# Kernel optimization log

Measured on AMD Instinct MI355X. Metric: run time of the kernel, lower is better.

## Reference

```python
import jax, jax.numpy as jnp
import numpy as np

D_MODEL = 1024
NUM_HEADS = 16
HEAD_DIM = D_MODEL // NUM_HEADS  # 64


def setup_inputs() -> dict:
    key = jax.random.key(0)
    ks = jax.random.split(key, 9)
    s = 1.0 / np.sqrt(D_MODEL)
    return {
        "x": jax.random.normal(ks[0], (2, 2048, D_MODEL), dtype=jnp.float32),
        "Wq": jax.random.normal(ks[1], (D_MODEL, D_MODEL), dtype=jnp.float32) * s,
        "bq": jnp.zeros((D_MODEL,), dtype=jnp.float32),
        "Wk": jax.random.normal(ks[2], (D_MODEL, HEAD_DIM), dtype=jnp.float32) * s,
        "bk": jnp.zeros((HEAD_DIM,), dtype=jnp.float32),
        "Wv": jax.random.normal(ks[3], (D_MODEL, HEAD_DIM), dtype=jnp.float32) * s,
        "bv": jnp.zeros((HEAD_DIM,), dtype=jnp.float32),
        "Wo": jax.random.normal(ks[4], (D_MODEL, D_MODEL), dtype=jnp.float32) * s,
        "bo": jnp.zeros((D_MODEL,), dtype=jnp.float32),
    }


def reference(x, Wq, bq, Wk, bk, Wv, bv, Wo, bo):
    B, S, D = x.shape
    H, hd = NUM_HEADS, HEAD_DIM
    # Projections: Q has H heads, K/V a single shared head (MQA).
    Q = (x @ Wq + bq).reshape(B, S, H, hd).transpose(0, 2, 1, 3)  # [B,H,S,hd]
    K = x @ Wk + bk  # [B,S,hd]
    V = x @ Wv + bv  # [B,S,hd]
    # Shared-K/V attention: broadcast K across heads instead of expand().
    scores = jnp.einsum("bhqd,bkd->bhqk", Q, K) / np.sqrt(hd)  # [B,H,S,S]
    attn = jax.nn.softmax(scores, axis=-1)
    attended = jnp.einsum("bhqk,bkd->bhqd", attn, V)  # [B,H,S,hd]
    attended = attended.transpose(0, 2, 1, 3).reshape(B, S, D)
    return attended @ Wo + bo
```

## Files before the change

kernel.cpp:

```cpp
#include <hip/hip_runtime.h>
#include <hip/hip_bf16.h>

#define D_MODEL 1024
#define NHEADS  16
#define HD      64
#define BATCH   2
#define SEQ     2048
#define MROWS   4096
#define NQKV    1152
#define NSPLIT  2

typedef short  short4v __attribute__((ext_vector_type(4)));
typedef short  short8  __attribute__((ext_vector_type(8)));
typedef float  floatx4 __attribute__((ext_vector_type(4)));

__device__ inline short f2bf(float f) {
  unsigned u = __builtin_bit_cast(unsigned, f);
  u = (u + 0x7FFF + ((u >> 16) & 1)) >> 16;
  return (short)u;
}

__device__ inline unsigned pack_trunc(float lo, float hi) {
  return __builtin_amdgcn_perm(__builtin_bit_cast(unsigned, hi),
                               __builtin_bit_cast(unsigned, lo), 0x07060302u);
}

__device__ inline void async_copy16(const short* g, short* l) {
  __builtin_amdgcn_global_load_lds(
      (const __attribute__((address_space(1))) unsigned int*)g,
      (__attribute__((address_space(3))) unsigned int*)l, 16, 0, 0);
}

__global__ __launch_bounds__(256)
void prep_kernel(const float* __restrict__ x,  const float* __restrict__ Wq,
                 const float* __restrict__ Wk, const float* __restrict__ Wv,
                 const float* __restrict__ Wo, const float* __restrict__ bq,
                 const float* __restrict__ bk, const float* __restrict__ bv,
                 short* __restrict__ xb, short* __restrict__ Wqkv_t,
                 short* __restrict__ Wo_t, float* __restrict__ bqkv) {
  const int id = blockIdx.x;
  const int t  = threadIdx.x;
  if (id < 544) {
    __shared__ short Ts[64 * 72];
    const float* src; short* dst; int N, off, tile;
    if (id < 256)      { src = Wq; dst = Wqkv_t; N = 1024; off = 0;    tile = id; }
    else if (id < 272) { src = Wk; dst = Wqkv_t; N = 64;   off = 1024; tile = id - 256; }
    else if (id < 288) { src = Wv; dst = Wqkv_t; N = 64;   off = 1088; tile = id - 272; }
    else               { src = Wo; dst = Wo_t;   N = 1024; off = 0;    tile = id - 288; }
    const int k0 = (N == 1024) ? (tile & 15) * 64 : tile * 64;
    const int n0 = (N == 1024) ? (tile >> 4) * 64 : 0;
    {
      const int r = t >> 2, c = (t & 3) * 16;
      const float* s = src + (size_t)(k0 + r) * N + n0 + c;
#pragma unroll
      for (int j = 0; j < 16; j += 4) {
        float4 v = *reinterpret_cast<const float4*>(s + j);
        Ts[r * 72 + c + j + 0] = f2bf(v.x); Ts[r * 72 + c + j + 1] = f2bf(v.y);
        Ts[r * 72 + c + j + 2] = f2bf(v.z); Ts[r * 72 + c + j + 3] = f2bf(v.w);
      }
    }
    __syncthreads();
    {
      const int n = t >> 2, kc = (t & 3) * 16;
      short8 o0, o1;
#pragma unroll
      for (int j = 0; j < 8; ++j) o0[j] = Ts[(kc + j) * 72 + n];
#pragma unroll
      for (int j = 0; j < 8; ++j) o1[j] = Ts[(kc + 8 + j) * 72 + n];
      short* d = dst + (size_t)(off + n0 + n) * 1024 + k0 + kc;
      *reinterpret_cast<short8*>(d)     = o0;
      *reinterpret_cast<short8*>(d + 8) = o1;
    }
  } else if (id < 549) {
    const int i = (id - 544) * 256 + t;
    if (i < 1024)      bqkv[i] = bq[i];
    else if (i < 1088) bqkv[i] = bk[i - 1024];
    else if (i < 1152) bqkv[i] = bv[i - 1088];
  } else {
    const int i = ((id - 549) * 256 + t) * 8;
    if (i < MROWS * D_MODEL) {
      float4 a = *reinterpret_cast<const float4*>(x + i);
      float4 b = *reinterpret_cast<const float4*>(x + i + 4);
      short8 o;
      o[0] = f2bf(a.x); o[1] = f2bf(a.y); o[2] = f2bf(a.z); o[3] = f2bf(a.w);
      o[4] = f2bf(b.x); o[5] = f2bf(b.y); o[6] = f2bf(b.z); o[7] = f2bf(b.w);
      *reinterpret_cast<short8*>(xb + i) = o;
    }
  }
}

template<bool OUT_BF16, int SCALE_N, bool VT_FUSE>
__global__ __launch_bounds__(256)
void gemm_mfma_bt(const short* __restrict__ A, const short* __restrict__ Bt,
                  const float* __restrict__ bias, void* __restrict__ Cout,
                  short* __restrict__ Vtg, int M, int N, int K) {
  __shared__ short As[128 * 64];
  __shared__ short Bs[64 * 64];
  const int t    = threadIdx.x;
  const int w    = t >> 6;
  const int lane = t & 63;
  const int quad = lane >> 4;
  const int l16  = lane & 15;
  const int bm   = blockIdx.x * 128;
  const int bn   = blockIdx.y * 64;
  const int wm   = (w >> 1) * 64;
  const int wn   = (w & 1) * 32;

  const int srow = t >> 3;
  const int cc   = ((t & 7) ^ (srow & 7)) * 8;
  const short* gA = A  + (size_t)(bm + srow) * K + cc;
  const short* gB = Bt + (size_t)(bn + srow) * K + cc;
  short* lA = As + t * 8;
  short* lB = Bs + t * 8;

  floatx4 acc[4][2];
#pragma unroll
  for (int i = 0; i < 4; ++i)
#pragma unroll
    for (int j = 0; j < 2; ++j) acc[i][j] = (floatx4){0.f, 0.f, 0.f, 0.f};

  const int xr = l16 & 7;

  for (int k0 = 0; k0 < K; k0 += 64) {
    __syncthreads();
    async_copy16(gA + k0, lA);
    async_copy16(gA + (size_t)32 * K + k0, lA + 2048);
    async_copy16(gA + (size_t)64 * K + k0, lA + 4096);
    async_copy16(gA + (size_t)96 * K + k0, lA + 6144);
    async_copy16(gB + k0, lB);
    async_copy16(gB + (size_t)32 * K + k0, lB + 2048);
    __syncthreads();

    short8 fa0[4], fa1[4], fb0[2], fb1[2];
#pragma unroll
    for (int mi = 0; mi < 4; ++mi) {
      const int row = wm + mi * 16 + l16;
      fa0[mi] = *reinterpret_cast<const short8*>(&As[row * 64 + (quad ^ xr) * 8]);
      fa1[mi] = *reinterpret_cast<const short8*>(&As[row * 64 + ((4 + quad) ^ xr) * 8]);
    }
#pragma unroll
    for (int ni = 0; ni < 2; ++ni) {
      const int row = wn + ni * 16 + l16;
      fb0[ni] = *reinterpret_cast<const short8*>(&Bs[row * 64 + (quad ^ xr) * 8]);
      fb1[ni] = *reinterpret_cast<const short8*>(&Bs[row * 64 + ((4 + quad) ^ xr) * 8]);
    }
#pragma unroll
    for (int mi = 0; mi < 4; ++mi)
#pragma unroll
      for (int ni = 0; ni < 2; ++ni) {
        acc[mi][ni] = __builtin_amdgcn_mfma_f32_16x16x32_bf16(fa0[mi], fb0[ni], acc[mi][ni], 0, 0, 0);
        acc[mi][ni] = __builtin_amdgcn_mfma_f32_16x16x32_bf16(fa1[mi], fb1[ni], acc[mi][ni], 0, 0, 0);
      }
  }

#pragma unroll
  for (int ni = 0; ni < 2; ++ni) {
    const int col = bn + wn + ni * 16 + l16;
    const float bs = bias[col];
    const float sc = (col < SCALE_N) ? 0.18033688f : 1.0f;
#pragma unroll
    for (int mi = 0; mi < 4; ++mi) {
      const int row = bm + wm + mi * 16 + quad * 4;
      short4v vt4;
#pragma unroll
      for (int r = 0; r < 4; ++r) {
        const float v = (acc[mi][ni][r] + bs) * sc;
        if (OUT_BF16) {
          const short bv16 = f2bf(v);
          ((short*)Cout)[(size_t)(row + r) * N + col] = bv16;
          if (VT_FUSE) vt4[r] = bv16;
        } else {
          ((float*)Cout)[(size_t)(row + r) * N + col] = v;
        }
      }
      if (VT_FUSE && col >= 1088) {
        const int d = col - 1088;
        const int b = row >> 11, s = row & 2047;
        *reinterpret_cast<short4v*>(&Vtg[(size_t)(b * 64 + d) * SEQ + s]) = vt4;
      }
    }
  }
}

__global__ __launch_bounds__(256, 3)
void mqa_flash_bf16(const short* __restrict__ QKV, const short* __restrict__ Vtg,
                    _Float16* __restrict__ Opart, float* __restrict__ lpart) {
  const int bh    = blockIdx.y;
  const int b     = bh >> 4;
  const int h     = bh & 15;
  const int s0    = blockIdx.x * 128;
  const int split = blockIdx.z;
  const int t     = threadIdx.x;
  const int w     = t >> 6;
  const int lane  = t & 63;
  const int quad  = lane >> 4;
  const int l16   = lane & 15;

  __shared__ short KVs[16384];
  __shared__ short Ps[4 * 16 * 64];
  short* myPs = Ps + w * 1024;

  short8 aq[2][2];
#pragma unroll
  for (int st = 0; st < 2; ++st) {
    const short* qrow = &QKV[(size_t)(b * SEQ + s0 + w * 32 + st * 16 + l16) * NQKV + h * HD];
    aq[st][0] = *reinterpret_cast<const short8*>(qrow + quad * 8);
    aq[st][1] = *reinterpret_cast<const short8*>(qrow + 32 + quad * 8);
  }

  floatx4 oacc[2][4];
  floatx4 lacc[2];
#pragma unroll
  for (int st = 0; st < 2; ++st) {
    lacc[st] = (floatx4){0.f, 0.f, 0.f, 0.f};
#pragma unroll
    for (int dg = 0; dg < 4; ++dg) oacc[st][dg] = (floatx4){0.f, 0.f, 0.f, 0.f};
  }

  short8 ones;
#pragma unroll
  for (int j = 0; j < 8; ++j) ones[j] = (short)0x3F80;

  const int srow  = t >> 3;
  const int cc    = ((t & 7) ^ (srow & 7)) * 8;
  const int kbase = split * (SEQ / NSPLIT);
  const short* gK = QKV + (size_t)(b * SEQ + kbase + srow) * NQKV + 1024 + cc;
  const short* gV = Vtg + (size_t)(b * 64 + srow) * SEQ + kbase + cc;
  short* lK = KVs + w * 512;
  short* lV = KVs + 4096 + w * 512;

  const int xr = l16 & 7;

  async_copy16(gK, lK);
  async_copy16(gK + (size_t)32 * NQKV, lK + 2048);
  async_copy16(gV, lV);
  async_copy16(gV + (size_t)32 * SEQ, lV + 2048);
  gK += (size_t)64 * NQKV;
  gV += 64;

  const int NT = (SEQ / NSPLIT) / 64;
  int cur = 0;

  for (int it = 0; it < NT; ++it) {
    asm volatile("s_waitcnt vmcnt(0)" ::: "memory");
    __builtin_amdgcn_s_barrier();
    __builtin_amdgcn_sched_barrier(0);

    if (it + 1 < NT) {
      const int nb = (cur ^ 1) * 8192;
      async_copy16(gK, lK + nb);
      async_copy16(gK + (size_t)32 * NQKV, lK + nb + 2048);
      async_copy16(gV, lV + nb);
      async_copy16(gV + (size_t)32 * SEQ, lV + nb + 2048);
      gK += (size_t)64 * NQKV;
      gV += 64;
    }

    const short* Ks = KVs + cur * 8192;
    const short* Vt = Ks + 4096;

    short8 kb[4][2], vb[4][2];
#pragma unroll
    for (int kg = 0; kg < 4; ++kg) {
      kb[kg][0] = *reinterpret_cast<const short8*>(&Ks[(kg * 16 + l16) * 64 + (quad ^ xr) * 8]);
      kb[kg][1] = *reinterpret_cast<const short8*>(&Ks[(kg * 16 + l16) * 64 + ((4 + quad) ^ xr) * 8]);
    }
#pragma unroll
    for (int dg = 0; dg < 4; ++dg) {
      vb[dg][0] = *reinterpret_cast<const short8*>(&Vt[(dg * 16 + l16) * 64 + (quad ^ xr) * 8]);
      vb[dg][1] = *reinterpret_cast<const short8*>(&Vt[(dg * 16 + l16) * 64 + ((4 + quad) ^ xr) * 8]);
    }
    asm volatile("s_waitcnt lgkmcnt(0)" ::: "memory");
    __builtin_amdgcn_sched_barrier(0);

#pragma unroll
    for (int st = 0; st < 2; ++st) {
#pragma unroll
      for (int kg = 0; kg < 4; ++kg) {
        floatx4 s4 = (floatx4){0.f, 0.f, 0.f, 0.f};
        s4 = __builtin_amdgcn_mfma_f32_16x16x32_bf16(kb[kg][0], aq[st][0], s4, 0, 0, 0);
        s4 = __builtin_amdgcn_mfma_f32_16x16x32_bf16(kb[kg][1], aq[st][1], s4, 0, 0, 0);
        float p0 = __builtin_exp2f(s4[0]);
        float p1 = __builtin_exp2f(s4[1]);
        float p2 = __builtin_exp2f(s4[2]);
        float p3 = __builtin_exp2f(s4[3]);
        uint2 pk;
        pk.x = pack_trunc(p0, p1);
        pk.y = pack_trunc(p2, p3);
        *reinterpret_cast<uint2*>(
            &myPs[l16 * 64 + (((2 * kg + (quad >> 1)) ^ xr) * 8) + (quad & 1) * 4]) = pk;
      }
      short8 ap0 = *reinterpret_cast<const short8*>(&myPs[l16 * 64 + ((quad ^ xr) * 8)]);
      short8 ap1 = *reinterpret_cast<const short8*>(&myPs[l16 * 64 + (((4 + quad) ^ xr) * 8)]);
      __builtin_amdgcn_s_setprio(1);
      lacc[st] = __builtin_amdgcn_mfma_f32_16x16x32_bf16(ap0, ones, lacc[st], 0, 0, 0);
      lacc[st] = __builtin_amdgcn_mfma_f32_16x16x32_bf16(ap1, ones, lacc[st], 0, 0, 0);
#pragma unroll
      for (int dg = 0; dg < 4; ++dg) {
        oacc[st][dg] = __builtin_amdgcn_mfma_f32_16x16x32_bf16(ap0, vb[dg][0], oacc[st][dg], 0, 0, 0);
        oacc[st][dg] = __builtin_amdgcn_mfma_f32_16x16x32_bf16(ap1, vb[dg][1], oacc[st][dg], 0, 0, 0);
      }
      __builtin_amdgcn_s_setprio(0);
    }
    cur ^= 1;
  }

#pragma unroll
  for (int st = 0; st < 2; ++st) {
#pragma unroll
    for (int rg = 0; rg < 4; ++rg) {
      const int qg = s0 + w * 32 + st * 16 + quad * 4 + rg;
      _Float16* dst = Opart + ((size_t)(split * 32 + bh) * SEQ + qg) * 64 + l16;
#pragma unroll
      for (int dg = 0; dg < 4; ++dg) dst[dg * 16] = (_Float16)oacc[st][dg][rg];
      if (l16 == 0) lpart[(size_t)(split * 32 + bh) * SEQ + qg] = lacc[st][rg];
    }
  }
}

__global__ __launch_bounds__(256)
void combine_kernel(const _Float16* __restrict__ Opart, const float* __restrict__ lpart,
                    short* __restrict__ Att) {
  const int idx = blockIdx.x * 256 + threadIdx.x;
  const int r   = idx >> 3;
  const int d0  = (idx & 7) * 8;
  float l = 0.f;
  float o[8] = {0.f,0.f,0.f,0.f,0.f,0.f,0.f,0.f};
#pragma unroll
  for (int s = 0; s < NSPLIT; ++s) {
    const _Float16* op = Opart + ((size_t)(s * 32 * SEQ) + r) * 64 + d0;
    l += lpart[(size_t)s * 32 * SEQ + r];
#pragma unroll
    for (int j = 0; j < 8; ++j) o[j] += (float)op[j];
  }
  const float inv = 1.0f / l;
  short8 ov;
#pragma unroll
  for (int j = 0; j < 8; ++j) ov[j] = f2bf(o[j] * inv);
  const int bhh = r >> 11, q = r & 2047;
  const int bb = bhh >> 4, hh = bhh & 15;
  *reinterpret_cast<short8*>(&Att[(size_t)(bb * SEQ + q) * D_MODEL + hh * HD + d0]) = ov;
}

extern "C" void kernel_launch(void* const* d_in, const int* in_sizes, int n_in,
                              void* d_out, int out_size, void* d_ws, size_t ws_size,
                              hipStream_t stream) {
  const float* x  = (const float*)d_in[0];
  const float* Wq = (const float*)d_in[1];
  const float* bq = (const float*)d_in[2];
  const float* Wk = (const float*)d_in[3];
  const float* bk = (const float*)d_in[4];
  const float* Wv = (const float*)d_in[5];
  const float* bv = (const float*)d_in[6];
  const float* Wo = (const float*)d_in[7];
  const float* bo = (const float*)d_in[8];
  float* out = (float*)d_out;

  short* Wqkv_t = (short*)d_ws;
  short* Wo_t   = Wqkv_t + (size_t)NQKV * D_MODEL;
  short* xb     = Wo_t + (size_t)D_MODEL * D_MODEL;
  short* QKV    = xb + (size_t)MROWS * D_MODEL;
  short* Att    = QKV + (size_t)MROWS * NQKV;
  short* Vtg    = Att + (size_t)MROWS * D_MODEL;
  float* bqkv   = (float*)(Vtg + (size_t)BATCH * HD * SEQ);
  float* lpart  = bqkv + 1152;
  _Float16* Opart = (_Float16*)(lpart + (size_t)NSPLIT * 32 * SEQ);

  prep_kernel<<<2597, 256, 0, stream>>>(x, Wq, Wk, Wv, Wo, bq, bk, bv,
                                        xb, Wqkv_t, Wo_t, bqkv);

  gemm_mfma_bt<true, 1024, true><<<dim3(MROWS / 128, NQKV / 64), 256, 0, stream>>>(
      xb, Wqkv_t, bqkv, QKV, Vtg, MROWS, NQKV, D_MODEL);

  mqa_flash_bf16<<<dim3(SEQ / 128, BATCH * NHEADS, NSPLIT), 256, 0, stream>>>(
      QKV, Vtg, Opart, lpart);

  combine_kernel<<<2048, 256, 0, stream>>>(Opart, lpart, Att);

  gemm_mfma_bt<false, 0, false><<<dim3(MROWS / 128, D_MODEL / 64), 256, 0, stream>>>(
      Att, Wo_t, bo, out, nullptr, MROWS, D_MODEL, D_MODEL);
}
```

Before: 185.0 us.

## Drop split-K attention and combine kernel; keep P in registers via permuted K rows

Removes the two-way key split and the separate combine kernel, so each block walks the full sequence and writes the normalized bf16 output straight into the attention buffer. K rows are loaded in a permuted order so that the MFMA score output layout lines up with the A-operand layout of the next MFMA. This lets exp2'd probabilities be packed in registers instead of going through an LDS round trip. The trade-off is half as many blocks (512) and longer per-block loops, which reduces parallelism and latency hiding.

Measured after the change: 172.2 us. -6.9%, faster.

```diff
diff --git a/kernel.cpp b/kernel.cpp
--- a/kernel.cpp
+++ b/kernel.cpp
@@ -8,11 +8,11 @@
 #define SEQ     2048
 #define MROWS   4096
 #define NQKV    1152
-#define NSPLIT  2
 
 typedef short  short4v __attribute__((ext_vector_type(4)));
 typedef short  short8  __attribute__((ext_vector_type(8)));
 typedef float  floatx4 __attribute__((ext_vector_type(4)));
+typedef unsigned uint4v __attribute__((ext_vector_type(4)));
 
 __device__ inline short f2bf(float f) {
   unsigned u = __builtin_bit_cast(unsigned, f);
@@ -184,12 +184,11 @@
 
 __global__ __launch_bounds__(256, 3)
 void mqa_flash_bf16(const short* __restrict__ QKV, const short* __restrict__ Vtg,
-                    _Float16* __restrict__ Opart, float* __restrict__ lpart) {
+                    short* __restrict__ Att) {
   const int bh    = blockIdx.y;
   const int b     = bh >> 4;
   const int h     = bh & 15;
   const int s0    = blockIdx.x * 128;
-  const int split = blockIdx.z;
   const int t     = threadIdx.x;
   const int w     = t >> 6;
   const int lane  = t & 63;
@@ -197,8 +196,6 @@
   const int l16   = lane & 15;
 
   __shared__ short KVs[16384];
-  __shared__ short Ps[4 * 16 * 64];
-  short* myPs = Ps + w * 1024;
 
   short8 aq[2][2];
 #pragma unroll
@@ -221,11 +218,11 @@
 #pragma unroll
   for (int j = 0; j < 8; ++j) ones[j] = (short)0x3F80;
 
-  const int srow  = t >> 3;
-  const int cc    = ((t & 7) ^ (srow & 7)) * 8;
-  const int kbase = split * (SEQ / NSPLIT);
-  const short* gK = QKV + (size_t)(b * SEQ + kbase + srow) * NQKV + 1024 + cc;
-  const short* gV = Vtg + (size_t)(b * 64 + srow) * SEQ + kbase + cc;
+  const int srow = t >> 3;
+  const int cc   = ((t & 7) ^ (srow & 7)) * 8;
+  const int krow = ((srow >> 4) & 1) * 4 + ((srow >> 2) & 3) * 8 + (srow & 3);
+  const short* gK = QKV + (size_t)(b * SEQ + krow) * NQKV + 1024 + cc;
+  const short* gV = Vtg + (size_t)(b * 64 + srow) * SEQ + cc;
   short* lK = KVs + w * 512;
   short* lV = KVs + 4096 + w * 512;
 
@@ -238,7 +235,7 @@
   gK += (size_t)64 * NQKV;
   gV += 64;
 
-  const int NT = (SEQ / NSPLIT) / 64;
+  const int NT = SEQ / 64;
   int cur = 0;
 
   for (int it = 0; it < NT; ++it) {
@@ -275,23 +272,28 @@
 
 #pragma unroll
     for (int st = 0; st < 2; ++st) {
+      floatx4 s4[4];
 #pragma unroll
       for (int kg = 0; kg < 4; ++kg) {
-        floatx4 s4 = (floatx4){0.f, 0.f, 0.f, 0.f};
-        s4 = __builtin_amdgcn_mfma_f32_16x16x32_bf16(kb[kg][0], aq[st][0], s4, 0, 0, 0);
-        s4 = __builtin_amdgcn_mfma_f32_16x16x32_bf16(kb[kg][1], aq[st][1], s4, 0, 0, 0);
-        float p0 = __builtin_exp2f(s4[0]);
-        float p1 = __builtin_exp2f(s4[1]);
-        float p2 = __builtin_exp2f(s4[2]);
-        float p3 = __builtin_exp2f(s4[3]);
-        uint2 pk;
-        pk.x = pack_trunc(p0, p1);
-        pk.y = pack_trunc(p2, p3);
-        *reinterpret_cast<uint2*>(
-            &myPs[l16 * 64 + (((2 * kg + (quad >> 1)) ^ xr) * 8) + (quad & 1) * 4]) = pk;
-      }
-      short8 ap0 = *reinterpret_cast<const short8*>(&myPs[l16 * 64 + ((quad ^ xr) * 8)]);
-      short8 ap1 = *reinterpret_cast<const short8*>(&myPs[l16 * 64 + (((4 + quad) ^ xr) * 8)]);
+        s4[kg] = (floatx4){0.f, 0.f, 0.f, 0.f};
+        s4[kg] = __builtin_amdgcn_mfma_f32_16x16x32_bf16(kb[kg][0], aq[st][0], s4[kg], 0, 0, 0);
+        s4[kg] = __builtin_amdgcn_mfma_f32_16x16x32_bf16(kb[kg][1], aq[st][1], s4[kg], 0, 0, 0);
+      }
+      unsigned pk[8];
+#pragma unroll
+      for (int kg = 0; kg < 4; ++kg) {
+        const float p0 = __builtin_exp2f(s4[kg][0]);
+        const float p1 = __builtin_exp2f(s4[kg][1]);
+        const float p2 = __builtin_exp2f(s4[kg][2]);
+        const float p3 = __builtin_exp2f(s4[kg][3]);
+        pk[kg * 2 + 0] = pack_trunc(p0, p1);
+        pk[kg * 2 + 1] = pack_trunc(p2, p3);
+      }
+      const uint4v u0 = (uint4v){pk[0], pk[1], pk[2], pk[3]};
+      const uint4v u1 = (uint4v){pk[4], pk[5], pk[6], pk[7]};
+      const short8 ap0 = __builtin_bit_cast(short8, u0);
+      const short8 ap1 = __builtin_bit_cast(short8, u1);
+
       __builtin_amdgcn_s_setprio(1);
       lacc[st] = __builtin_amdgcn_mfma_f32_16x16x32_bf16(ap0, ones, lacc[st], 0, 0, 0);
       lacc[st] = __builtin_amdgcn_mfma_f32_16x16x32_bf16(ap1, ones, lacc[st], 0, 0, 0);
@@ -305,41 +307,18 @@
     cur ^= 1;
   }
 
+  short* At = Att + (size_t)b * SEQ * D_MODEL + h * HD;
 #pragma unroll
   for (int st = 0; st < 2; ++st) {
 #pragma unroll
     for (int rg = 0; rg < 4; ++rg) {
-      const int qg = s0 + w * 32 + st * 16 + quad * 4 + rg;
-      _Float16* dst = Opart + ((size_t)(split * 32 + bh) * SEQ + qg) * 64 + l16;
-#pragma unroll
-      for (int dg = 0; dg < 4; ++dg) dst[dg * 16] = (_Float16)oacc[st][dg][rg];
-      if (l16 == 0) lpart[(size_t)(split * 32 + bh) * SEQ + qg] = lacc[st][rg];
-    }
-  }
-}
-
-__global__ __launch_bounds__(256)
-void combine_kernel(const _Float16* __restrict__ Opart, const float* __restrict__ lpart,
-                    short* __restrict__ Att) {
-  const int idx = blockIdx.x * 256 + threadIdx.x;
-  const int r   = idx >> 3;
-  const int d0  = (idx & 7) * 8;
-  float l = 0.f;
-  float o[8] = {0.f,0.f,0.f,0.f,0.f,0.f,0.f,0.f};
-#pragma unroll
-  for (int s = 0; s < NSPLIT; ++s) {
-    const _Float16* op = Opart + ((size_t)(s * 32 * SEQ) + r) * 64 + d0;
-    l += lpart[(size_t)s * 32 * SEQ + r];
-#pragma unroll
-    for (int j = 0; j < 8; ++j) o[j] += (float)op[j];
-  }
-  const float inv = 1.0f / l;
-  short8 ov;
-#pragma unroll
-  for (int j = 0; j < 8; ++j) ov[j] = f2bf(o[j] * inv);
-  const int bhh = r >> 11, q = r & 2047;
-  const int bb = bhh >> 4, hh = bhh & 15;
-  *reinterpret_cast<short8*>(&Att[(size_t)(bb * SEQ + q) * D_MODEL + hh * HD + d0]) = ov;
+      const int q = s0 + w * 32 + st * 16 + quad * 4 + rg;
+      const float inv = 1.0f / lacc[st][rg];
+      short* dst = At + (size_t)q * D_MODEL + l16;
+#pragma unroll
+      for (int dg = 0; dg < 4; ++dg) dst[dg * 16] = f2bf(oacc[st][dg][rg] * inv);
+    }
+  }
 }
 
 extern "C" void kernel_launch(void* const* d_in, const int* in_sizes, int n_in,
@@ -363,8 +342,6 @@
   short* Att    = QKV + (size_t)MROWS * NQKV;
   short* Vtg    = Att + (size_t)MROWS * D_MODEL;
   float* bqkv   = (float*)(Vtg + (size_t)BATCH * HD * SEQ);
-  float* lpart  = bqkv + 1152;
-  _Float16* Opart = (_Float16*)(lpart + (size_t)NSPLIT * 32 * SEQ);
 
   prep_kernel<<<2597, 256, 0, stream>>>(x, Wq, Wk, Wv, Wo, bq, bk, bv,
                                         xb, Wqkv_t, Wo_t, bqkv);
@@ -372,10 +349,8 @@
   gemm_mfma_bt<true, 1024, true><<<dim3(MROWS / 128, NQKV / 64), 256, 0, stream>>>(
       xb, Wqkv_t, bqkv, QKV, Vtg, MROWS, NQKV, D_MODEL);
 
-  mqa_flash_bf16<<<dim3(SEQ / 128, BATCH * NHEADS, NSPLIT), 256, 0, stream>>>(
-      QKV, Vtg, Opart, lpart);
-
-  combine_kernel<<<2048, 256, 0, stream>>>(Opart, lpart, Att);
+  mqa_flash_bf16<<<dim3(SEQ / 128, BATCH * NHEADS), 256, 0, stream>>>(
+      QKV, Vtg, Att);
 
   gemm_mfma_bt<false, 0, false><<<dim3(MROWS / 128, D_MODEL / 64), 256, 0, stream>>>(
       Att, Wo_t, bo, out, nullptr, MROWS, D_MODEL, D_MODEL);
```

## Keep softmax probabilities in registers by permuting K rows to match MFMA layout

Applied to the files above, without the earlier changes.

Removes the per-wave LDS scratch buffer used to transpose the exp'd score tile into the A-operand layout of the PV MFMA. K rows are loaded into shared memory in a permuted order, so each lane's score accumulator outputs already line up with the key positions it needs as A-operand for P·V. The packed bf16 values are then fed straight from registers. This drops LDS writes, reads and waits in the inner loop, and frees LDS that may allow higher occupancy. It relies on the row permutation being consistent for both the QK and PV contractions.

Result: faster. 174.9 us (-5.5%).

```diff
diff --git a/kernel.cpp b/kernel.cpp
--- a/kernel.cpp
+++ b/kernel.cpp
@@ -13,6 +13,7 @@
 typedef short  short4v __attribute__((ext_vector_type(4)));
 typedef short  short8  __attribute__((ext_vector_type(8)));
 typedef float  floatx4 __attribute__((ext_vector_type(4)));
+typedef unsigned uint4v __attribute__((ext_vector_type(4)));
 
 __device__ inline short f2bf(float f) {
   unsigned u = __builtin_bit_cast(unsigned, f);
@@ -197,8 +198,6 @@
   const int l16   = lane & 15;
 
   __shared__ short KVs[16384];
-  __shared__ short Ps[4 * 16 * 64];
-  short* myPs = Ps + w * 1024;
 
   short8 aq[2][2];
 #pragma unroll
@@ -223,8 +222,9 @@
 
   const int srow  = t >> 3;
   const int cc    = ((t & 7) ^ (srow & 7)) * 8;
+  const int krow  = ((srow >> 4) & 1) * 4 + ((srow >> 2) & 3) * 8 + (srow & 3);
   const int kbase = split * (SEQ / NSPLIT);
-  const short* gK = QKV + (size_t)(b * SEQ + kbase + srow) * NQKV + 1024 + cc;
+  const short* gK = QKV + (size_t)(b * SEQ + kbase + krow) * NQKV + 1024 + cc;
   const short* gV = Vtg + (size_t)(b * 64 + srow) * SEQ + kbase + cc;
   short* lK = KVs + w * 512;
   short* lV = KVs + 4096 + w * 512;
@@ -275,23 +275,28 @@
 
 #pragma unroll
     for (int st = 0; st < 2; ++st) {
+      floatx4 s4[4];
 #pragma unroll
       for (int kg = 0; kg < 4; ++kg) {
-        floatx4 s4 = (floatx4){0.f, 0.f, 0.f, 0.f};
-        s4 = __builtin_amdgcn_mfma_f32_16x16x32_bf16(kb[kg][0], aq[st][0], s4, 0, 0, 0);
-        s4 = __builtin_amdgcn_mfma_f32_16x16x32_bf16(kb[kg][1], aq[st][1], s4, 0, 0, 0);
-        float p0 = __builtin_exp2f(s4[0]);
-        float p1 = __builtin_exp2f(s4[1]);
-        float p2 = __builtin_exp2f(s4[2]);
-        float p3 = __builtin_exp2f(s4[3]);
-        uint2 pk;
-        pk.x = pack_trunc(p0, p1);
-        pk.y = pack_trunc(p2, p3);
-        *reinterpret_cast<uint2*>(
-            &myPs[l16 * 64 + (((2 * kg + (quad >> 1)) ^ xr) * 8) + (quad & 1) * 4]) = pk;
-      }
-      short8 ap0 = *reinterpret_cast<const short8*>(&myPs[l16 * 64 + ((quad ^ xr) * 8)]);
-      short8 ap1 = *reinterpret_cast<const short8*>(&myPs[l16 * 64 + (((4 + quad) ^ xr) * 8)]);
+        s4[kg] = (floatx4){0.f, 0.f, 0.f, 0.f};
+        s4[kg] = __builtin_amdgcn_mfma_f32_16x16x32_bf16(kb[kg][0], aq[st][0], s4[kg], 0, 0, 0);
+        s4[kg] = __builtin_amdgcn_mfma_f32_16x16x32_bf16(kb[kg][1], aq[st][1], s4[kg], 0, 0, 0);
+      }
+      unsigned pk[8];
+#pragma unroll
+      for (int kg = 0; kg < 4; ++kg) {
+        const float p0 = __builtin_exp2f(s4[kg][0]);
+        const float p1 = __builtin_exp2f(s4[kg][1]);
+        const float p2 = __builtin_exp2f(s4[kg][2]);
+        const float p3 = __builtin_exp2f(s4[kg][3]);
+        pk[kg * 2 + 0] = pack_trunc(p0, p1);
+        pk[kg * 2 + 1] = pack_trunc(p2, p3);
+      }
+      const uint4v u0 = (uint4v){pk[0], pk[1], pk[2], pk[3]};
+      const uint4v u1 = (uint4v){pk[4], pk[5], pk[6], pk[7]};
+      const short8 ap0 = __builtin_bit_cast(short8, u0);
+      const short8 ap1 = __builtin_bit_cast(short8, u1);
+
       __builtin_amdgcn_s_setprio(1);
       lacc[st] = __builtin_amdgcn_mfma_f32_16x16x32_bf16(ap0, ones, lacc[st], 0, 0, 0);
       lacc[st] = __builtin_amdgcn_mfma_f32_16x16x32_bf16(ap1, ones, lacc[st], 0, 0, 0);
```
